# Performance work log

Hardware: AMD Instinct MI355X
Metric: run time of the kernel (lower is better)

Reference implementation:

```python
import jax, jax.numpy as jnp
import numpy as np
import math

H = 8          # num_heads
DH = 16        # dim_head
DEPTH = 1
LAMBDA_INIT = 0.8 - 0.6 * math.exp(-0.3 * DEPTH)
LN_EPS = 1e-5


def setup_inputs() -> dict:
    key = jax.random.key(0)
    ks = jax.random.split(key, 12)
    dim = 256
    inner = 2 * H * DH  # 256
    b, n = 2, 2048
    s = lambda fan_in: 1.0 / math.sqrt(fan_in)
    return {
        "x": jax.random.normal(ks[0], (b, n, dim), jnp.float32),
        "Wq": jax.random.normal(ks[1], (dim, inner), jnp.float32) * s(dim),
        "Wkv": jax.random.normal(ks[2], (dim, 2 * inner), jnp.float32) * s(dim),
        "Wout": jax.random.normal(ks[3], (inner, dim), jnp.float32) * s(inner),
        "bout": jnp.zeros((dim,), jnp.float32),
        "Wg": jax.random.normal(ks[4], (dim, inner), jnp.float32) * s(dim),
        "bg": jnp.ones((inner,), jnp.float32),
        "lq1": jax.random.normal(ks[5], (DH,), jnp.float32) * 0.1,
        "lk1": jax.random.normal(ks[6], (DH,), jnp.float32) * 0.1,
        "lq2": jax.random.normal(ks[7], (DH,), jnp.float32) * 0.1,
        "lk2": jax.random.normal(ks[8], (DH,), jnp.float32) * 0.1,
        "ln_gamma": jnp.ones((2 * DH,), jnp.float32),
        "ln_beta": jnp.zeros((2 * DH,), jnp.float32),
    }


def reference(x, Wq, Wkv, Wout, bout, Wg, bg, lq1, lk1, lq2, lk2, ln_gamma, ln_beta):
    b, n, dim = x.shape
    scale = DH ** (-0.5)

    q = x @ Wq                                   # [b, n, 2*H*DH]
    kv = x @ Wkv                                 # [b, n, 4*H*DH]
    k, v = jnp.split(kv, 2, axis=-1)

    # doubled heads for q, k; normal heads with width 2*DH for v
    q = q.reshape(b, n, 2 * H, DH).transpose(0, 2, 1, 3) * scale  # [b, 2H, n, DH]
    k = k.reshape(b, n, 2 * H, DH).transpose(0, 2, 1, 3)          # [b, 2H, n, DH]
    v = v.reshape(b, n, H, 2 * DH).transpose(0, 2, 1, 3)          # [b, H, n, 2DH]

    dots = jnp.einsum('bhid,bhjd->bhij', q, k)   # [b, 2H, n, n]
    attn = jax.nn.softmax(dots, axis=-1)

    lam1 = jnp.exp(jnp.sum(lq1 * lk1))
    lam2 = jnp.exp(jnp.sum(lq2 * lk2))
    lam = lam1 - lam2 + LAMBDA_INIT

    attn = attn.reshape(b, H, 2, n, n)
    attn = attn[:, :, 0] - lam * attn[:, :, 1]   # [b, H, n, n]

    out = jnp.einsum('bhij,bhjd->bhid', attn, v)  # [b, H, n, 2DH]

    # LayerNorm over last dim (2*DH)
    mu = jnp.mean(out, axis=-1, keepdims=True)
    var = jnp.var(out, axis=-1, keepdims=True)
    out = (out - mu) * jax.lax.rsqrt(var + LN_EPS) * ln_gamma + ln_beta

    out = out * (1.0 - LAMBDA_INIT)
    out = out.transpose(0, 2, 1, 3).reshape(b, n, H * 2 * DH)  # [b, n, inner]

    gates = x @ Wg + bg
    out = out * jax.nn.sigmoid(gates)
    return out @ Wout + bout
```

## Files before the change

### kernel.cpp

```cpp
#include <hip/hip_runtime.h>
#include <hip/hip_bf16.h>

#define LAMBDA_INIT_F 0.35550906759096927f
#define ONE_MINUS_LI  0.64449093240903073f
#define QSCALE 0.36067376022224085f

typedef unsigned short u16;
typedef unsigned int   u32;
typedef short s4v  __attribute__((ext_vector_type(4)));
typedef float f16v __attribute__((ext_vector_type(16)));

__device__ __forceinline__ u16 f2bf(float f) {
    __hip_bfloat16 h = __float2bfloat16(f);
    return *reinterpret_cast<u16*>(&h);
}
__device__ __forceinline__ u32 pk2bf(float lo, float hi) {
    return (u32)f2bf(lo) | ((u32)f2bf(hi) << 16);
}
union U2S { u32 u[2]; s4v s; };
__device__ __forceinline__ s4v mks4(u32 a, u32 b) { U2S x; x.u[0]=a; x.u[1]=b; return x.s; }

__device__ __forceinline__ float fexp2(float x) {
#if __has_builtin(__builtin_amdgcn_exp2f)
    return __builtin_amdgcn_exp2f(x);
#else
    float r; asm volatile("v_exp_f32 %0, %1\n\ts_nop 1" : "=v"(r) : "v"(x)); return r;
#endif
}

#define MFMA(a,b,c) __builtin_amdgcn_mfma_f32_32x32x8bf16_1k((a),(b),(c),0,0,0)

__global__ __launch_bounds__(256) void prep_kernel(
    const float* __restrict__ Wq, const float* __restrict__ Wkv,
    const float* __restrict__ Wg, const float* __restrict__ Wout,
    const float* __restrict__ x,
    u16* __restrict__ WT, u16* __restrict__ xbf)
{
    const int bid = blockIdx.x;
    const int tid = threadIdx.x;

    if (bid >= 80) {
        const int r0 = (bid - 80) * 64;
        const float2* src = (const float2*)(x + (size_t)r0 * 256);
        u32* dst = (u32*)(xbf + (size_t)r0 * 256);
        for (int idx = tid; idx < 64 * 128; idx += 256) {
            float2 v = src[idx];
            dst[idx] = pk2bf(v.x, v.y);
        }
        return;
    }

    __shared__ u16 tile[16 * 258];
    const int n0g = bid * 16;
    const float* src; int cols; int ncol0;
    if      (n0g < 256)  { src = Wq;   cols = 256; ncol0 = n0g; }
    else if (n0g < 768)  { src = Wkv;  cols = 512; ncol0 = n0g - 256; }
    else if (n0g < 1024) { src = Wg;   cols = 256; ncol0 = n0g - 768; }
    else                 { src = Wout; cols = 256; ncol0 = n0g - 1024; }

    const float* srow = src + (size_t)tid * cols + ncol0;
#pragma unroll
    for (int j = 0; j < 8; ++j) {
        const float2 v = *(const float2*)(srow + 2*j);
        tile[(2*j + 0) * 258 + tid] = f2bf(v.x);
        tile[(2*j + 1) * 258 + tid] = f2bf(v.y);
    }
    __syncthreads();

    const u32* t32 = (const u32*)tile;
    const int nn = tid >> 4, part = tid & 15;
    u32* dst = (u32*)WT + (size_t)(n0g + nn) * 128 + part * 8;
    const u32* s2 = t32 + nn * 129 + part * 8;
#pragma unroll
    for (int j = 0; j < 8; ++j) dst[j] = s2[j];
}

__global__ __launch_bounds__(256) void proj_kernel(
    const u16* __restrict__ x, const u16* __restrict__ WT,
    const float* __restrict__ bg,
    u16* __restrict__ Qb, u16* __restrict__ Kb,
    u16* __restrict__ Vb, float* __restrict__ Gb)
{
    const int bid = blockIdx.x;
    const int nt = bid & 15, mt = bid >> 4;
    const int tid = threadIdx.x, w = tid >> 6, lane = tid & 63;
    const int l31 = lane & 31, hh = lane >> 5;
    const int m0 = mt * 128 + w * 32;
    const int n0 = nt * 64;

    const u16* xr  = x  + (size_t)(m0 + l31) * 256 + 4*hh;
    const u16* br0 = WT + (size_t)(n0 + l31) * 256 + 4*hh;
    const u16* br1 = WT + (size_t)(n0 + 32 + l31) * 256 + 4*hh;

    f16v a0, a1;
#pragma unroll
    for (int r = 0; r < 16; ++r) { a0[r] = 0.f; a1[r] = 0.f; }

#pragma unroll
    for (int ks = 0; ks < 16; ++ks) {
        s4v xa  = *(const s4v*)(xr  + ks*16);
        s4v xb  = *(const s4v*)(xr  + ks*16 + 8);
        s4v w0a = *(const s4v*)(br0 + ks*16);
        s4v w0b = *(const s4v*)(br0 + ks*16 + 8);
        s4v w1a = *(const s4v*)(br1 + ks*16);
        s4v w1b = *(const s4v*)(br1 + ks*16 + 8);
        a0 = MFMA(xa, w0a, a0); a0 = MFMA(xb, w0b, a0);
        a1 = MFMA(xa, w1a, a1); a1 = MFMA(xb, w1b, a1);
    }

    const int cat = nt >> 2;
#pragma unroll
    for (int ns = 0; ns < 2; ++ns) {
        const f16v& acc = ns ? a1 : a0;
        const int n = nt * 64 + ns * 32 + l31;
#pragma unroll
        for (int r = 0; r < 16; ++r) {
            const int il = (r & 3) + 8*(r >> 2) + 4*hh;
            const int R = m0 + il;
            const int b = R >> 11, i = R & 2047;
            const float v = acc[r];
            if (cat == 0) {
                const int h = n >> 4, d = n & 15;
                Qb[((size_t)(b*16 + h) * 2048 + i) * 16 + d] = f2bf(v * QSCALE);
            } else if (cat == 1) {
                const int nk = n - 256, h = nk >> 4, d = nk & 15;
                Kb[((size_t)(b*16 + h) * 2048 + i) * 16 + d] = f2bf(v);
            } else if (cat == 2) {
                const int nv = n - 512, hv = nv >> 5, d2 = nv & 31;
                Vb[((size_t)(b*8 + hv) * 2048 + i) * 32 + d2] = f2bf(v);
            } else {
                const int gcol = n - 768;
                const float t = v + bg[gcol];
                Gb[(size_t)R * 256 + gcol] = 1.0f / (1.0f + __expf(-t));
            }
        }
    }
}

__global__ __launch_bounds__(512, 8) void attn_kernel(
    const u16* __restrict__ Q, const u16* __restrict__ K,
    const u16* __restrict__ V, const float* __restrict__ G,
    const float* __restrict__ lq1, const float* __restrict__ lk1,
    const float* __restrict__ lq2, const float* __restrict__ lk2,
    const float* __restrict__ gamma, const float* __restrict__ beta,
    u16* __restrict__ A)
{
    __shared__ float smemf[8960];
    u16* st  = (u16*)smemf;
    u32* stu = (u32*)smemf;

    const int bid = blockIdx.x;
    const int itile = bid & 63;
    const int combo = bid >> 6;
    const int ho = combo & 7, b = combo >> 3;
    const int i0 = itile * 32;

    const int tid = threadIdx.x, w = tid >> 6, lane = tid & 63;
    const int l31 = lane & 31, hh = lane >> 5;
    const int s = w & 1, jq = w >> 1;

    const u16* Vg = V + (size_t)(b*8 + ho) * 2048 * 32;
    const u16* Qg = Q + ((size_t)(b*16 + 2*ho + s) * 2048 + (i0 + l31)) * 16;
    const s4v qf0 = *(const s4v*)(Qg + 4*hh);
    const s4v qf1 = *(const s4v*)(Qg + 8 + 4*hh);

    const int qp = tid >> 7;
    const int pid = tid & 127;
    const int ksub = pid >> 6, krow = (pid >> 1) & 31, kseg = pid & 1;
    const u32* kgp = (const u32*)(K + (size_t)(b*16 + 2*ho + ksub) * 2048 * 16)
                     + (size_t)qp * 4096 + krow * 8 + kseg * 4;
    const int vj = pid >> 2, vseg = pid & 3;
    const u32* vgp = (const u32*)Vg + (size_t)qp * 8192 + vj * 16 + vseg * 4;

    const int kw_off = qp*1120 + ksub*288 + krow*9 + kseg*4;
    const int vw_u16 = qp*2240 + 1152 + vj;
    const int vd0 = vseg * 8;
    const int kr_off = jq*1120 + s*288 + l31*9 + 2*hh;
    const int vr_off = jq*1120 + 576 + l31*17;

    f16v oacc;
#pragma unroll
    for (int r = 0; r < 16; ++r) oacc[r] = 0.f;
    float la0 = 0.f, la1 = 0.f;

    {
        u32 k0 = kgp[0], k1 = kgp[1], k2 = kgp[2], k3 = kgp[3];
        u32 v0 = vgp[0], v1 = vgp[1], v2 = vgp[2], v3 = vgp[3];
        u32* kd = stu + kw_off;
        kd[0]=k0; kd[1]=k1; kd[2]=k2; kd[3]=k3;
        u16* vd = st + vw_u16;
        vd[(vd0+0)*34] = (u16)(v0 & 0xffff); vd[(vd0+1)*34] = (u16)(v0 >> 16);
        vd[(vd0+2)*34] = (u16)(v1 & 0xffff); vd[(vd0+3)*34] = (u16)(v1 >> 16);
        vd[(vd0+4)*34] = (u16)(v2 & 0xffff); vd[(vd0+5)*34] = (u16)(v2 >> 16);
        vd[(vd0+6)*34] = (u16)(v3 & 0xffff); vd[(vd0+7)*34] = (u16)(v3 >> 16);
    }

    for (int t = 0; t < 16; ++t) {
        __syncthreads();
        const int p = t & 1, pn = 1 - p;
        const int tt = (t + 1) & 15;

        const u32* kp = kgp + (size_t)tt * 256;
        u32 nk0=kp[0], nk1=kp[1], nk2=kp[2], nk3=kp[3];
        const u32* vp = vgp + (size_t)tt * 512;
        u32 nv0=vp[0], nv1=vp[1], nv2=vp[2], nv3=vp[3];

        const u32* kb2 = stu + p*4480 + kr_off;
        const u32* vb2 = stu + p*4480 + vr_off;

        f16v sc;
#pragma unroll
        for (int r = 0; r < 16; ++r) sc[r] = 0.f;
        {
            s4v kf0 = mks4(kb2[0], kb2[1]);
            sc = MFMA(kf0, qf0, sc);
            s4v kf1 = mks4(kb2[4], kb2[5]);
            sc = MFMA(kf1, qf1, sc);
        }
        float pv[16];
#pragma unroll
        for (int r = 0; r < 16; ++r) pv[r] = fexp2(sc[r]);
        la0 += pv[0];  la0 += pv[1];  la0 += pv[2];  la0 += pv[3];
        la1 += pv[4];  la1 += pv[5];  la1 += pv[6];  la1 += pv[7];
        la0 += pv[8];  la0 += pv[9];  la0 += pv[10]; la0 += pv[11];
        la1 += pv[12]; la1 += pv[13]; la1 += pv[14]; la1 += pv[15];
#pragma unroll
        for (int f = 0; f < 4; ++f) {
            u32 plo = __builtin_amdgcn_perm(__float_as_uint(pv[4*f+1]),
                                            __float_as_uint(pv[4*f+0]), 0x07060302);
            u32 phi = __builtin_amdgcn_perm(__float_as_uint(pv[4*f+3]),
                                            __float_as_uint(pv[4*f+2]), 0x07060302);
            s4v pf = mks4(plo, phi);
            s4v vf = mks4(vb2[4*f + 2*hh], vb2[4*f + 2*hh + 1]);
            oacc = MFMA(pf, vf, oacc);
        }

        {
            u32* kd = stu + pn*4480 + kw_off;
            kd[0]=nk0; kd[1]=nk1; kd[2]=nk2; kd[3]=nk3;
            u16* vd = st + pn*8960 + vw_u16;
            vd[(vd0+0)*34] = (u16)(nv0 & 0xffff); vd[(vd0+1)*34] = (u16)(nv0 >> 16);
            vd[(vd0+2)*34] = (u16)(nv1 & 0xffff); vd[(vd0+3)*34] = (u16)(nv1 >> 16);
            vd[(vd0+4)*34] = (u16)(nv2 & 0xffff); vd[(vd0+5)*34] = (u16)(nv2 >> 16);
            vd[(vd0+6)*34] = (u16)(nv3 & 0xffff); vd[(vd0+7)*34] = (u16)(nv3 >> 16);
        }
    }
    const float lacc = la0 + la1;

    __syncthreads();
    float ltot = lacc + __shfl_xor(lacc, 32);
    float* ob = smemf + w * 1056;
#pragma unroll
    for (int r = 0; r < 16; ++r) {
        const int il = (r & 3) + 8*(r >> 2) + 4*hh;
        ob[il*33 + l31] = oacc[r];
    }
    if (lane < 32) smemf[8448 + w*32 + l31] = ltot;
    __syncthreads();

    if (tid < 32) {
        const int ii = tid;
        float l1 = 0.f, l2 = 0.f;
#pragma unroll
        for (int q = 0; q < 4; ++q) {
            l1 += smemf[8448 + (2*q + 0)*32 + ii];
            l2 += smemf[8448 + (2*q + 1)*32 + ii];
        }

        float sA = 0.f, sB = 0.f;
#pragma unroll
        for (int d = 0; d < 16; ++d) {
            sA += lq1[d] * lk1[d];
            sB += lq2[d] * lk2[d];
        }
        const float lam = __expf(sA) - __expf(sB) + LAMBDA_INIT_F;
        const float c1 = 1.f / l1, c2 = lam / l2;

        float od[32], mu = 0.f;
#pragma unroll
        for (int d = 0; d < 32; ++d) {
            float o1 = 0.f, o2 = 0.f;
#pragma unroll
            for (int q = 0; q < 4; ++q) {
                o1 += smemf[(2*q + 0)*1056 + ii*33 + d];
                o2 += smemf[(2*q + 1)*1056 + ii*33 + d];
            }
            od[d] = o1 * c1 - o2 * c2;
            mu += od[d];
        }
        mu *= (1.f / 32.f);
        float var = 0.f;
#pragma unroll
        for (int d = 0; d < 32; ++d) { const float t2 = od[d] - mu; var += t2 * t2; }
        var *= (1.f / 32.f);
        const float rs = rsqrtf(var + 1e-5f);

        const int R = b*2048 + i0 + ii;
        const float* Gr = G + (size_t)R * 256 + ho*32;
        u16* Ar = A + (size_t)R * 256 + ho*32;
#pragma unroll
        for (int d = 0; d < 32; ++d) {
            const float val = (od[d] - mu)*rs*gamma[d] + beta[d];
            Ar[d] = f2bf(val * ONE_MINUS_LI * Gr[d]);
        }
    }
}

__global__ __launch_bounds__(512) void out_kernel(
    const u16* __restrict__ Abf, const u16* __restrict__ WT,
    const float* __restrict__ bout, float* __restrict__ out)
{
    __shared__ float cs[4][32 * 33];

    const int bid = blockIdx.x;
    const int nt = bid & 3, mt = bid >> 2;
    const int tid = threadIdx.x, w = tid >> 6, lane = tid & 63;
    const int l31 = lane & 31, hh = lane >> 5;
    const int t = w >> 1, kh = w & 1;
    const int m0 = mt * 64 + (t & 1) * 32;
    const int n0 = nt * 64 + (t >> 1) * 32;

    const u16* ar = Abf + (size_t)(m0 + l31) * 256 + kh*128 + 4*hh;
    const u16* br = WT + (size_t)(1024 + n0 + l31) * 256 + kh*128 + 4*hh;

    f16v acc;
#pragma unroll
    for (int r = 0; r < 16; ++r) acc[r] = 0.f;

#pragma unroll
    for (int ks = 0; ks < 8; ++ks) {
        s4v aa = *(const s4v*)(ar + ks*16);
        s4v ab = *(const s4v*)(ar + ks*16 + 8);
        s4v ba = *(const s4v*)(br + ks*16);
        s4v bb = *(const s4v*)(br + ks*16 + 8);
        acc = MFMA(aa, ba, acc);
        acc = MFMA(ab, bb, acc);
    }

    if (kh == 0) {
#pragma unroll
        for (int r = 0; r < 16; ++r) {
            const int il = (r & 3) + 8*(r >> 2) + 4*hh;
            cs[t][il*33 + l31] = acc[r];
        }
    }
    __syncthreads();
    if (kh == 1) {
        const float bv = bout[n0 + l31];
#pragma unroll
        for (int r = 0; r < 16; ++r) {
            const int il = (r & 3) + 8*(r >> 2) + 4*hh;
            const int m = m0 + il;
            out[(size_t)m * 256 + n0 + l31] = acc[r] + cs[t][il*33 + l31] + bv;
        }
    }
}

extern "C" void kernel_launch(void* const* d_in, const int* in_sizes, int n_in,
                              void* d_out, int out_size, void* d_ws, size_t ws_size,
                              hipStream_t stream) {
    const float* x    = (const float*)d_in[0];
    const float* Wq   = (const float*)d_in[1];
    const float* Wkv  = (const float*)d_in[2];
    const float* Wout = (const float*)d_in[3];
    const float* bout = (const float*)d_in[4];
    const float* Wg   = (const float*)d_in[5];
    const float* bg   = (const float*)d_in[6];
    const float* lq1  = (const float*)d_in[7];
    const float* lk1  = (const float*)d_in[8];
    const float* lq2  = (const float*)d_in[9];
    const float* lk2  = (const float*)d_in[10];
    const float* lng  = (const float*)d_in[11];
    const float* lnb  = (const float*)d_in[12];

    u16*   WT  = (u16*)d_ws;
    u16*   xbf = WT + 327680;
    u16*   Qb  = xbf + 1048576;
    u16*   Kb  = Qb + 1048576;
    u16*   Vb  = Kb + 1048576;
    float* Gb  = (float*)(Vb + 1048576);
    u16*   Abf = (u16*)(Gb + 1048576);

    hipLaunchKernelGGL(prep_kernel, dim3(144), dim3(256), 0, stream,
                       Wq, Wkv, Wg, Wout, x, WT, xbf);
    hipLaunchKernelGGL(proj_kernel, dim3(512), dim3(256), 0, stream,
                       xbf, WT, bg, Qb, Kb, Vb, Gb);
    hipLaunchKernelGGL(attn_kernel, dim3(1024), dim3(512), 0, stream,
                       Qb, Kb, Vb, Gb, lq1, lk1, lq2, lk2, lng, lnb, Abf);
    hipLaunchKernelGGL(out_kernel, dim3(256), dim3(512), 0, stream,
                       Abf, WT, bout, (float*)d_out);
}
```

Before: 159.7 us.

## Switch to 32x32x16 bf16 MFMA with permlane32 swaps and parallel epilogue

Replaces the 32x32x8 bf16 MFMA with the gfx950 32x32x16 instruction in the projection, attention and output kernels, so each lane loads 8 bf16 values per operand and half as many MFMA issues are needed. In the attention P·V step it repacks P into the new operand layout using permlane32_swap. The attention epilogue now spreads each row across 4 threads, combining partial LayerNorm sums with shuffles and writing with vectorized loads and stores, instead of using 32 serial threads. This relies on the permlane swap producing the correct k-ordering for the wider MFMA operand layout.

```diff
diff --git a/kernel.cpp b/kernel.cpp
--- a/kernel.cpp
+++ b/kernel.cpp
@@ -8,6 +8,8 @@
 typedef unsigned short u16;
 typedef unsigned int   u32;
 typedef short s4v  __attribute__((ext_vector_type(4)));
+typedef short s8v  __attribute__((ext_vector_type(8)));
+typedef u32   u32x4 __attribute__((ext_vector_type(4)));
 typedef float f16v __attribute__((ext_vector_type(16)));
 
 __device__ __forceinline__ u16 f2bf(float f) {
@@ -17,8 +19,10 @@
 __device__ __forceinline__ u32 pk2bf(float lo, float hi) {
     return (u32)f2bf(lo) | ((u32)f2bf(hi) << 16);
 }
-union U2S { u32 u[2]; s4v s; };
-__device__ __forceinline__ s4v mks4(u32 a, u32 b) { U2S x; x.u[0]=a; x.u[1]=b; return x.s; }
+union U4S8 { u32 u[4]; s8v s; };
+__device__ __forceinline__ s8v mks8(u32 a, u32 b, u32 c, u32 d) {
+    U4S8 x; x.u[0]=a; x.u[1]=b; x.u[2]=c; x.u[3]=d; return x.s;
+}
 
 __device__ __forceinline__ float fexp2(float x) {
 #if __has_builtin(__builtin_amdgcn_exp2f)
@@ -28,7 +32,12 @@
 #endif
 }
 
-#define MFMA(a,b,c) __builtin_amdgcn_mfma_f32_32x32x8bf16_1k((a),(b),(c),0,0,0)
+#define MFMA16(a,b,c) __builtin_amdgcn_mfma_f32_32x32x16_bf16((a),(b),(c),0,0,0)
+
+__device__ __forceinline__ void plswap2(u32& a, u32& b) {
+    auto r = __builtin_amdgcn_permlane32_swap(a, b, false, false);
+    a = r[0]; b = r[1];
+}
 
 __global__ __launch_bounds__(256) void prep_kernel(
     const float* __restrict__ Wq, const float* __restrict__ Wkv,
@@ -88,9 +97,9 @@
     const int m0 = mt * 128 + w * 32;
     const int n0 = nt * 64;
 
-    const u16* xr  = x  + (size_t)(m0 + l31) * 256 + 4*hh;
-    const u16* br0 = WT + (size_t)(n0 + l31) * 256 + 4*hh;
-    const u16* br1 = WT + (size_t)(n0 + 32 + l31) * 256 + 4*hh;
+    const u16* xr  = x  + (size_t)(m0 + l31) * 256 + 8*hh;
+    const u16* br0 = WT + (size_t)(n0 + l31) * 256 + 8*hh;
+    const u16* br1 = WT + (size_t)(n0 + 32 + l31) * 256 + 8*hh;
 
     f16v a0, a1;
 #pragma unroll
@@ -98,14 +107,11 @@
 
 #pragma unroll
     for (int ks = 0; ks < 16; ++ks) {
-        s4v xa  = *(const s4v*)(xr  + ks*16);
-        s4v xb  = *(const s4v*)(xr  + ks*16 + 8);
-        s4v w0a = *(const s4v*)(br0 + ks*16);
-        s4v w0b = *(const s4v*)(br0 + ks*16 + 8);
-        s4v w1a = *(const s4v*)(br1 + ks*16);
-        s4v w1b = *(const s4v*)(br1 + ks*16 + 8);
-        a0 = MFMA(xa, w0a, a0); a0 = MFMA(xb, w0b, a0);
-        a1 = MFMA(xa, w1a, a1); a1 = MFMA(xb, w1b, a1);
+        s8v xa = *(const s8v*)(xr  + ks*16);
+        s8v w0 = *(const s8v*)(br0 + ks*16);
+        s8v w1 = *(const s8v*)(br1 + ks*16);
+        a0 = MFMA16(xa, w0, a0);
+        a1 = MFMA16(xa, w1, a1);
     }
 
     const int cat = nt >> 2;
@@ -161,8 +167,7 @@
 
     const u16* Vg = V + (size_t)(b*8 + ho) * 2048 * 32;
     const u16* Qg = Q + ((size_t)(b*16 + 2*ho + s) * 2048 + (i0 + l31)) * 16;
-    const s4v qf0 = *(const s4v*)(Qg + 4*hh);
-    const s4v qf1 = *(const s4v*)(Qg + 8 + 4*hh);
+    const s8v qf = *(const s8v*)(Qg + 8*hh);
 
     const int qp = tid >> 7;
     const int pid = tid & 127;
@@ -175,7 +180,7 @@
     const int kw_off = qp*1120 + ksub*288 + krow*9 + kseg*4;
     const int vw_u16 = qp*2240 + 1152 + vj;
     const int vd0 = vseg * 8;
-    const int kr_off = jq*1120 + s*288 + l31*9 + 2*hh;
+    const int kr_off = jq*1120 + s*288 + l31*9 + 4*hh;
     const int vr_off = jq*1120 + 576 + l31*17;
 
     f16v oacc;
@@ -212,10 +217,8 @@
 #pragma unroll
         for (int r = 0; r < 16; ++r) sc[r] = 0.f;
         {
-            s4v kf0 = mks4(kb2[0], kb2[1]);
-            sc = MFMA(kf0, qf0, sc);
-            s4v kf1 = mks4(kb2[4], kb2[5]);
-            sc = MFMA(kf1, qf1, sc);
+            s8v kf = mks8(kb2[0], kb2[1], kb2[2], kb2[3]);
+            sc = MFMA16(kf, qf, sc);
         }
         float pv[16];
 #pragma unroll
@@ -224,15 +227,23 @@
         la1 += pv[4];  la1 += pv[5];  la1 += pv[6];  la1 += pv[7];
         la0 += pv[8];  la0 += pv[9];  la0 += pv[10]; la0 += pv[11];
         la1 += pv[12]; la1 += pv[13]; la1 += pv[14]; la1 += pv[15];
-#pragma unroll
-        for (int f = 0; f < 4; ++f) {
-            u32 plo = __builtin_amdgcn_perm(__float_as_uint(pv[4*f+1]),
-                                            __float_as_uint(pv[4*f+0]), 0x07060302);
-            u32 phi = __builtin_amdgcn_perm(__float_as_uint(pv[4*f+3]),
-                                            __float_as_uint(pv[4*f+2]), 0x07060302);
-            s4v pf = mks4(plo, phi);
-            s4v vf = mks4(vb2[4*f + 2*hh], vb2[4*f + 2*hh + 1]);
-            oacc = MFMA(pf, vf, oacc);
+
+        u32 wv[8];
+#pragma unroll
+        for (int i = 0; i < 8; ++i)
+            wv[i] = __builtin_amdgcn_perm(__float_as_uint(pv[2*i+1]),
+                                          __float_as_uint(pv[2*i+0]), 0x07060302);
+        plswap2(wv[0], wv[2]); plswap2(wv[1], wv[3]);
+        {
+            s8v pf0 = mks8(wv[0], wv[1], wv[2], wv[3]);
+            s8v vf0 = mks8(vb2[4*hh+0], vb2[4*hh+1], vb2[4*hh+2], vb2[4*hh+3]);
+            oacc = MFMA16(pf0, vf0, oacc);
+        }
+        plswap2(wv[4], wv[6]); plswap2(wv[5], wv[7]);
+        {
+            s8v pf1 = mks8(wv[4], wv[5], wv[6], wv[7]);
+            s8v vf1 = mks8(vb2[8+4*hh+0], vb2[8+4*hh+1], vb2[8+4*hh+2], vb2[8+4*hh+3]);
+            oacc = MFMA16(pf1, vf1, oacc);
         }
 
         {
@@ -258,8 +269,8 @@
     if (lane < 32) smemf[8448 + w*32 + l31] = ltot;
     __syncthreads();
 
-    if (tid < 32) {
-        const int ii = tid;
+    if (tid < 128) {
+        const int ii = tid >> 2, sub = tid & 3, d0 = sub * 8;
         float l1 = 0.f, l2 = 0.f;
 #pragma unroll
         for (int q = 0; q < 4; ++q) {
@@ -276,33 +287,45 @@
         const float lam = __expf(sA) - __expf(sB) + LAMBDA_INIT_F;
         const float c1 = 1.f / l1, c2 = lam / l2;
 
-        float od[32], mu = 0.f;
-#pragma unroll
-        for (int d = 0; d < 32; ++d) {
+        float od[8]; float mu = 0.f;
+#pragma unroll
+        for (int dd = 0; dd < 8; ++dd) {
+            const int d = d0 + dd;
             float o1 = 0.f, o2 = 0.f;
 #pragma unroll
             for (int q = 0; q < 4; ++q) {
                 o1 += smemf[(2*q + 0)*1056 + ii*33 + d];
                 o2 += smemf[(2*q + 1)*1056 + ii*33 + d];
             }
-            od[d] = o1 * c1 - o2 * c2;
-            mu += od[d];
-        }
+            od[dd] = o1 * c1 - o2 * c2;
+            mu += od[dd];
+        }
+        mu += __shfl_xor(mu, 1); mu += __shfl_xor(mu, 2);
         mu *= (1.f / 32.f);
         float var = 0.f;
 #pragma unroll
-        for (int d = 0; d < 32; ++d) { const float t2 = od[d] - mu; var += t2 * t2; }
+        for (int dd = 0; dd < 8; ++dd) { const float t2 = od[dd] - mu; var += t2 * t2; }
+        var += __shfl_xor(var, 1); var += __shfl_xor(var, 2);
         var *= (1.f / 32.f);
         const float rs = rsqrtf(var + 1e-5f);
 
         const int R = b*2048 + i0 + ii;
-        const float* Gr = G + (size_t)R * 256 + ho*32;
-        u16* Ar = A + (size_t)R * 256 + ho*32;
-#pragma unroll
-        for (int d = 0; d < 32; ++d) {
-            const float val = (od[d] - mu)*rs*gamma[d] + beta[d];
-            Ar[d] = f2bf(val * ONE_MINUS_LI * Gr[d]);
-        }
+        const float* Gr = G + (size_t)R * 256 + ho*32 + d0;
+        const float4 g0 = *(const float4*)(Gr);
+        const float4 g1 = *(const float4*)(Gr + 4);
+        const float gg[8] = { g0.x, g0.y, g0.z, g0.w, g1.x, g1.y, g1.z, g1.w };
+        float vals[8];
+#pragma unroll
+        for (int dd = 0; dd < 8; ++dd) {
+            const float val = (od[dd] - mu)*rs*gamma[d0 + dd] + beta[d0 + dd];
+            vals[dd] = val * ONE_MINUS_LI * gg[dd];
+        }
+        u32x4 pk;
+        pk[0] = pk2bf(vals[0], vals[1]);
+        pk[1] = pk2bf(vals[2], vals[3]);
+        pk[2] = pk2bf(vals[4], vals[5]);
+        pk[3] = pk2bf(vals[6], vals[7]);
+        *reinterpret_cast<u32x4*>(A + (size_t)R * 256 + ho*32 + d0) = pk;
     }
 }
 
@@ -320,8 +343,8 @@
     const int m0 = mt * 64 + (t & 1) * 32;
     const int n0 = nt * 64 + (t >> 1) * 32;
 
-    const u16* ar = Abf + (size_t)(m0 + l31) * 256 + kh*128 + 4*hh;
-    const u16* br = WT + (size_t)(1024 + n0 + l31) * 256 + kh*128 + 4*hh;
+    const u16* ar = Abf + (size_t)(m0 + l31) * 256 + kh*128 + 8*hh;
+    const u16* br = WT + (size_t)(1024 + n0 + l31) * 256 + kh*128 + 8*hh;
 
     f16v acc;
 #pragma unroll
@@ -329,12 +352,9 @@
 
 #pragma unroll
     for (int ks = 0; ks < 8; ++ks) {
-        s4v aa = *(const s4v*)(ar + ks*16);
-        s4v ab = *(const s4v*)(ar + ks*16 + 8);
-        s4v ba = *(const s4v*)(br + ks*16);
-        s4v bb = *(const s4v*)(br + ks*16 + 8);
-        acc = MFMA(aa, ba, acc);
-        acc = MFMA(ab, bb, acc);
+        s8v aa = *(const s8v*)(ar + ks*16);
+        s8v ba = *(const s8v*)(br + ks*16);
+        acc = MFMA16(aa, ba, acc);
     }
 
     if (kh == 0) {
```

Result: faster. 141.5 us (-11.4%).
